# Kernel optimization log

Measured on AMD Instinct MI355X. Metric: run time of the kernel, lower is better.

## Reference

```python
import jax, jax.numpy as jnp
import numpy as np

MARGIN = 1.0


def setup_inputs() -> dict:
    key = jax.random.key(0)
    k1, k2, k3 = jax.random.split(key, 3)
    N, F = 4096, 512
    a = jax.random.normal(k1, (N, F), dtype=jnp.float32)
    b = jax.random.normal(k2, (N, F), dtype=jnp.float32)
    labels = jax.random.randint(k3, (N,), 0, 16, dtype=jnp.int32)
    return {"a": a, "b": b, "labels": labels}


def reference(a, b, labels):
    # D[i, j] = ||b_i - a_j||  (torch: Xa=a[None], Xb=b[:,None], sum over feat)
    # GEMM form of the pairwise sqdist; clamp tiny fp negatives before sqrt.
    Dsq = (jnp.sum(b * b, axis=1)[:, None]
           + jnp.sum(a * a, axis=1)[None, :]
           - 2.0 * (b @ a.T))
    D = jnp.sqrt(jnp.maximum(Dsq, 0.0))            # [N, N]
    Dexpm = jnp.exp(MARGIN - D)                    # [N, N]

    same = labels[:, None] == labels[None, :]      # [N, N]
    eye = jnp.eye(labels.shape[0], dtype=bool)
    pos_mask = same & ~eye                         # ordered positive pairs (i, j)
    neg_mask = ~same                               # negative pairs (labels differ)

    # neg_i sum for row i: sum_k Dexpm[i, k] over k with labels[k] != labels[i]
    row_negsum = jnp.sum(jnp.where(neg_mask, Dexpm, 0.0), axis=1)  # [N]

    # J_ij = log(neg_ik_sum + neg_jl_sum) + D[i, j]; hinged and squared
    J = jnp.log(row_negsum[:, None] + row_negsum[None, :]) + D
    hinge_sq = jnp.square(jnp.maximum(J, 0.0))

    num_pos = jnp.sum(pos_mask)
    return jnp.sum(jnp.where(pos_mask, hinge_sq, 0.0)) / (2.0 * num_pos)
```

## Files before the change

### kernel.cpp

```cpp
#include <hip/hip_runtime.h>
#include <math.h>

#define NROW 4096
#define FDIM 512
#define MARGIN 1.0f

typedef __attribute__((ext_vector_type(8))) short short8;
typedef __attribute__((ext_vector_type(4))) float floatx4;

__device__ inline unsigned short f2bf(float x) {
    unsigned u = __float_as_uint(x);
    return (unsigned short)((u + 0x7FFFu + ((u >> 16) & 1u)) >> 16);
}
__device__ inline float h2f(unsigned short u) {
    _Float16 h; __builtin_memcpy(&h, &u, 2); return (float)h;
}
__device__ inline unsigned short f2h(float f) {
    _Float16 h = (_Float16)f; unsigned short u; __builtin_memcpy(&u, &h, 2); return u;
}
__device__ inline void glds16(const unsigned short* g, unsigned short* l) {
    __builtin_amdgcn_global_load_lds(
        (const __attribute__((address_space(1))) unsigned int*)g,
        (__attribute__((address_space(3))) unsigned int*)l, 16, 0, 0);
}

__global__ __launch_bounds__(64) void prep_kernel(
    const float* __restrict__ a, const float* __restrict__ b,
    unsigned short* __restrict__ abf, unsigned short* __restrict__ bbf,
    float* __restrict__ na, float* __restrict__ nb,
    float* __restrict__ rns, float* __restrict__ loss) {
    int row  = blockIdx.x;
    int lane = threadIdx.x;
    const float4* a4 = (const float4*)(a + (size_t)row * FDIM);
    const float4* b4 = (const float4*)(b + (size_t)row * FDIM);
    ushort4* au = (ushort4*)(abf + (size_t)row * FDIM);
    ushort4* bu = (ushort4*)(bbf + (size_t)row * FDIM);
    float sa = 0.f, sb = 0.f;
    #pragma unroll
    for (int f = lane; f < FDIM / 4; f += 64) {
        float4 va = a4[f];
        float4 vb = b4[f];
        sa += va.x * va.x + va.y * va.y + va.z * va.z + va.w * va.w;
        sb += vb.x * vb.x + vb.y * vb.y + vb.z * vb.z + vb.w * vb.w;
        ushort4 ua = { f2bf(va.x), f2bf(va.y), f2bf(va.z), f2bf(va.w) };
        ushort4 ub = { f2bf(vb.x), f2bf(vb.y), f2bf(vb.z), f2bf(vb.w) };
        au[f] = ua;
        bu[f] = ub;
    }
    #pragma unroll
    for (int o = 32; o > 0; o >>= 1) {
        sa += __shfl_down(sa, o);
        sb += __shfl_down(sb, o);
    }
    if (lane == 0) {
        na[row] = sa;
        nb[row] = sb;
        rns[row] = 0.f;
        if (row == 0) loss[0] = 0.f;
    }
}

template <int MODE>
__global__ __launch_bounds__(256) void pass_mfma(
    const unsigned short* __restrict__ abf, const unsigned short* __restrict__ bbf,
    const int* __restrict__ labels,
    const float* __restrict__ na, const float* __restrict__ nb,
    float* __restrict__ rns, unsigned short* __restrict__ Dws,
    float* __restrict__ loss_sum)
{
    __shared__ __align__(16) unsigned short arena[16384];
    __shared__ int   li_s[128], lj_s[128];
    __shared__ float nb_s[128], na_s[128], rbi_s[128], rbj_s[128];

    const int t    = threadIdx.x;
    const int lane = t & 63;
    const int w    = t >> 6;
    const int wi   = w >> 1, wj = w & 1;
    const int bid  = blockIdx.x;
    const int sup  = bid >> 6, loc = bid & 63;
    const int by   = ((sup >> 2) << 3) | (loc >> 3);
    const int bx   = ((sup & 3) << 3) | (loc & 7);
    const int ti   = by * 128;
    const int tj   = bx * 128;
    const int lr   = lane & 15;
    const int lq   = lane >> 4;

    floatx4 acc[4][4];
    #pragma unroll
    for (int i = 0; i < 4; ++i)
        #pragma unroll
        for (int j = 0; j < 4; ++j)
            acc[i][j] = (floatx4){0.f, 0.f, 0.f, 0.f};

    if (t < 128) {
        li_s[t] = labels[ti + t];
        nb_s[t] = nb[ti + t];
        if (MODE == 2) rbi_s[t] = rns[ti + t];
    } else {
        int u = t - 128;
        lj_s[u] = labels[tj + u];
        na_s[u] = na[tj + u];
        if (MODE == 2) rbj_s[u] = rns[tj + u];
    }

    auto stage = [&](int kk, int buf) {
        unsigned short* As = arena + buf * 8192;
        unsigned short* Bs = arena + 4096 + buf * 8192;
        #pragma unroll
        for (int l = 0; l < 2; ++l) {
            int c   = t + l * 256;
            int row = c >> 2;
            int q   = c & 3;
            glds16(abf + (size_t)(tj + row) * FDIM + kk + q * 8, As + c * 8);
            glds16(bbf + (size_t)(ti + row) * FDIM + kk + q * 8, Bs + c * 8);
        }
    };

    stage(0, 0);
    __syncthreads();

    #pragma unroll
    for (int it = 0; it < FDIM / 32; ++it) {
        if (it < FDIM / 32 - 1) stage((it + 1) * 32, (it + 1) & 1);

        const unsigned short* As = arena + (it & 1) * 8192;
        const unsigned short* Bs = As + 4096;
        short8 af[4], bf[4];
        #pragma unroll
        for (int ri = 0; ri < 4; ++ri)
            af[ri] = *(const short8*)&Bs[(wi * 64 + ri * 16 + lr) * 32 + lq * 8];
        #pragma unroll
        for (int rj = 0; rj < 4; ++rj)
            bf[rj] = *(const short8*)&As[(wj * 64 + rj * 16 + lr) * 32 + lq * 8];
        #pragma unroll
        for (int ri = 0; ri < 4; ++ri)
            #pragma unroll
            for (int rj = 0; rj < 4; ++rj)
                acc[ri][rj] = __builtin_amdgcn_mfma_f32_16x16x32_bf16(
                    af[ri], bf[rj], acc[ri][rj], 0, 0, 0);
        __syncthreads();
    }

    if (MODE == 0 || MODE == 1) {
        unsigned short* dblk = Dws + (size_t)bid * 16384;
        #pragma unroll
        for (int ri = 0; ri < 4; ++ri) {
            float rs[4] = {0.f, 0.f, 0.f, 0.f};
            unsigned short dloc[16];
            #pragma unroll
            for (int rj = 0; rj < 4; ++rj) {
                int   jl  = wj * 64 + rj * 16 + lr;
                float naj = na_s[jl];
                int   ljv = lj_s[jl];
                #pragma unroll
                for (int r = 0; r < 4; ++r) {
                    int   il  = wi * 64 + ri * 16 + lq * 4 + r;
                    float dsq = nb_s[il] + naj - 2.f * acc[ri][rj][r];
                    float D   = sqrtf(fmaxf(dsq, 0.f));
                    if (li_s[il] != ljv) rs[r] += __expf(MARGIN - D);
                    if (MODE == 0) dloc[rj * 4 + r] = f2h(D);
                }
            }
            #pragma unroll
            for (int r = 0; r < 4; ++r) {
                #pragma unroll
                for (int o = 8; o > 0; o >>= 1) rs[r] += __shfl_down(rs[r], o, 16);
            }
            if (lr == 0) {
                #pragma unroll
                for (int r = 0; r < 4; ++r)
                    atomicAdd(&rns[ti + wi * 64 + ri * 16 + lq * 4 + r], rs[r]);
            }
            if (MODE == 0) {
                *(short8*)&dblk[(ri * 2 + 0) * 2048 + t * 8] = *(short8*)&dloc[0];
                *(short8*)&dblk[(ri * 2 + 1) * 2048 + t * 8] = *(short8*)&dloc[8];
            }
        }
    } else {
        float local = 0.f;
        #pragma unroll
        for (int ri = 0; ri < 4; ++ri)
            #pragma unroll
            for (int rj = 0; rj < 4; ++rj) {
                int jl  = wj * 64 + rj * 16 + lr;
                int ljv = lj_s[jl];
                float naj = na_s[jl], rbj = rbj_s[jl];
                #pragma unroll
                for (int r = 0; r < 4; ++r) {
                    int il = wi * 64 + ri * 16 + lq * 4 + r;
                    int i  = ti + il, j = tj + jl;
                    if (li_s[il] == ljv && i != j) {
                        float dsq = nb_s[il] + naj - 2.f * acc[ri][rj][r];
                        float D   = sqrtf(fmaxf(dsq, 0.f));
                        float J   = __logf(rbi_s[il] + rbj) + D;
                        float h   = fmaxf(J, 0.f);
                        local += h * h;
                    }
                }
            }
        #pragma unroll
        for (int o = 32; o > 0; o >>= 1) local += __shfl_down(local, o);
        __shared__ float part[4];
        if (lane == 0) part[w] = local;
        __syncthreads();
        if (t == 0) atomicAdd(loss_sum, part[0] + part[1] + part[2] + part[3]);
    }
}

__global__ __launch_bounds__(256) void pass2_sweep(
    const unsigned short* __restrict__ Dws, const int* __restrict__ labels,
    const float* __restrict__ rns, float* __restrict__ loss_sum)
{
    __shared__ int   lab_i[128], lab_j[128];
    __shared__ float rb_i[128], rb_j[128];

    const int t    = threadIdx.x;
    const int lane = t & 63;
    const int w    = t >> 6;
    const int wi   = w >> 1, wj = w & 1;
    const int bid  = blockIdx.x;
    const int sup  = bid >> 6, loc = bid & 63;
    const int by   = ((sup >> 2) << 3) | (loc >> 3);
    const int bx   = ((sup & 3) << 3) | (loc & 7);
    const int ti   = by * 128;
    const int tj   = bx * 128;
    const int lr   = lane & 15;
    const int lq   = lane >> 4;

    if (t < 128) {
        lab_i[t] = labels[ti + t];
        rb_i[t]  = rns[ti + t];
    } else {
        int u = t - 128;
        lab_j[u] = labels[tj + u];
        rb_j[u]  = rns[tj + u];
    }
    __syncthreads();

    const unsigned short* dblk = Dws + (size_t)bid * 16384;
    float local = 0.f;
    #pragma unroll
    for (int ri = 0; ri < 4; ++ri) {
        short8 d0 = *(const short8*)&dblk[(ri * 2 + 0) * 2048 + t * 8];
        short8 d1 = *(const short8*)&dblk[(ri * 2 + 1) * 2048 + t * 8];
        #pragma unroll
        for (int rj = 0; rj < 4; ++rj) {
            int jl  = wj * 64 + rj * 16 + lr;
            int ljv = lab_j[jl];
            #pragma unroll
            for (int r = 0; r < 4; ++r) {
                int il = wi * 64 + ri * 16 + lq * 4 + r;
                if (lab_i[il] == ljv && (ti + il) != (tj + jl)) {
                    unsigned short du = (rj < 2)
                        ? (unsigned short)d0[rj * 4 + r]
                        : (unsigned short)d1[(rj - 2) * 4 + r];
                    float J = __logf(rb_i[il] + rb_j[jl]) + h2f(du);
                    float h = fmaxf(J, 0.f);
                    local += h * h;
                }
            }
        }
    }
    #pragma unroll
    for (int o = 32; o > 0; o >>= 1) local += __shfl_down(local, o);
    __shared__ float part[4];
    if (lane == 0) part[w] = local;
    __syncthreads();
    if (t == 0) atomicAdd(loss_sum, part[0] + part[1] + part[2] + part[3]);
}

__global__ __launch_bounds__(256) void finalize_kernel(const int* __restrict__ labels,
                                                       const float* __restrict__ loss_sum,
                                                       float* __restrict__ out) {
    __shared__ int hist[16];
    int t = threadIdx.x;
    if (t < 16) hist[t] = 0;
    __syncthreads();
    for (int i = t; i < NROW; i += 256) atomicAdd(&hist[labels[i] & 15], 1);
    __syncthreads();
    if (t == 0) {
        long long np = 0;
        for (int c = 0; c < 16; ++c) np += (long long)hist[c] * (long long)(hist[c] - 1);
        out[0] = loss_sum[0] / (2.0f * (float)np);
    }
}

extern "C" void kernel_launch(void* const* d_in, const int* in_sizes, int n_in,
                              void* d_out, int out_size, void* d_ws, size_t ws_size,
                              hipStream_t stream) {
    const float* a      = (const float*)d_in[0];
    const float* b      = (const float*)d_in[1];
    const int*   labels = (const int*)d_in[2];
    float* out = (float*)d_out;

    unsigned short* abf = (unsigned short*)d_ws;
    unsigned short* bbf = abf + (size_t)NROW * FDIM;
    float* fws  = (float*)(bbf + (size_t)NROW * FDIM);
    float* na   = fws;
    float* nb   = fws + NROW;
    float* rns  = fws + 2 * NROW;
    float* loss = fws + 3 * NROW;
    unsigned short* Dws = (unsigned short*)(fws + 3 * NROW + 4);

    size_t need = ((char*)Dws - (char*)d_ws) + (size_t)NROW * NROW * 2;

    prep_kernel<<<NROW, 64, 0, stream>>>(a, b, abf, bbf, na, nb, rns, loss);

    dim3 grid((NROW / 128) * (NROW / 128));
    if (ws_size >= need) {
        pass_mfma<0><<<grid, 256, 0, stream>>>(abf, bbf, labels, na, nb, rns, Dws, loss);
        pass2_sweep<<<grid, 256, 0, stream>>>(Dws, labels, rns, loss);
    } else {
        pass_mfma<1><<<grid, 256, 0, stream>>>(abf, bbf, labels, na, nb, rns, Dws, loss);
        pass_mfma<2><<<grid, 256, 0, stream>>>(abf, bbf, labels, na, nb, rns, Dws, loss);
    }

    finalize_kernel<<<1, 256, 0, stream>>>(labels, loss, out);
}
```

Before: 135.1 us.

## Replace dense distance cache with label-grouped positive-pair GEMM pass

Stops writing the full fp16 distance matrix in the first pass and removes the dense second sweep. Rows are grouped by label (histogram plus permutation built in an extra prep block), and a work list of 64x64 same-label tiles is recomputed with a small MFMA GEMM over gathered rows. Only the roughly 1/16 of pairs that share a label are touched, and the last block folds in the finalize step. The cost is recomputing those dot products with a serial single-lane work-list build and gather-based loads.

```diff
diff --git a/kernel.cpp b/kernel.cpp
--- a/kernel.cpp
+++ b/kernel.cpp
@@ -4,6 +4,7 @@
 #define NROW 4096
 #define FDIM 512
 #define MARGIN 1.0f
+#define NLAB 16
 
 typedef __attribute__((ext_vector_type(8))) short short8;
 typedef __attribute__((ext_vector_type(4))) float floatx4;
@@ -11,12 +12,6 @@
 __device__ inline unsigned short f2bf(float x) {
     unsigned u = __float_as_uint(x);
     return (unsigned short)((u + 0x7FFFu + ((u >> 16) & 1u)) >> 16);
-}
-__device__ inline float h2f(unsigned short u) {
-    _Float16 h; __builtin_memcpy(&h, &u, 2); return (float)h;
-}
-__device__ inline unsigned short f2h(float f) {
-    _Float16 h = (_Float16)f; unsigned short u; __builtin_memcpy(&u, &h, 2); return u;
 }
 __device__ inline void glds16(const unsigned short* g, unsigned short* l) {
     __builtin_amdgcn_global_load_lds(
@@ -26,11 +21,50 @@
 
 __global__ __launch_bounds__(64) void prep_kernel(
     const float* __restrict__ a, const float* __restrict__ b,
+    const int* __restrict__ labels,
     unsigned short* __restrict__ abf, unsigned short* __restrict__ bbf,
     float* __restrict__ na, float* __restrict__ nb,
-    float* __restrict__ rns, float* __restrict__ loss) {
+    float* __restrict__ rns, float* __restrict__ loss,
+    int* __restrict__ perm, int* __restrict__ goff,
+    int* __restrict__ wl, int* __restrict__ wlmeta) {
     int row  = blockIdx.x;
     int lane = threadIdx.x;
+
+    if (row == NROW) {
+        __shared__ int hist[NLAB], off[NLAB], cur[NLAB];
+        if (lane < NLAB) hist[lane] = 0;
+        __syncthreads();
+        for (int i = lane; i < NROW; i += 64) atomicAdd(&hist[labels[i] & 15], 1);
+        __syncthreads();
+        if (lane == 0) {
+            int acc = 0;
+            for (int g = 0; g < NLAB; ++g) { off[g] = acc; acc += hist[g]; }
+            int n = 0;
+            int np = 0;
+            for (int g = 0; g < NLAB; ++g) {
+                goff[g] = off[g];
+                int c = hist[g];
+                np += c * (c - 1);
+                int nt = (c + 63) >> 6;
+                for (int ti = 0; ti < nt; ++ti)
+                    for (int tj = 0; tj < nt; ++tj)
+                        wl[n++] = (g << 12) | (ti << 6) | tj;
+            }
+            goff[NLAB] = NROW;
+            wlmeta[0] = n;
+            wlmeta[1] = np;
+            wlmeta[2] = 0;
+        }
+        __syncthreads();
+        if (lane < NLAB) cur[lane] = off[lane];
+        __syncthreads();
+        for (int i = lane; i < NROW; i += 64) {
+            int pos = atomicAdd(&cur[labels[i] & 15], 1);
+            perm[pos] = i;
+        }
+        return;
+    }
+
     const float4* a4 = (const float4*)(a + (size_t)row * FDIM);
     const float4* b4 = (const float4*)(b + (size_t)row * FDIM);
     ushort4* au = (ushort4*)(abf + (size_t)row * FDIM);
@@ -60,17 +94,15 @@
     }
 }
 
-template <int MODE>
-__global__ __launch_bounds__(256) void pass_mfma(
+__global__ __launch_bounds__(256) void pass_neg(
     const unsigned short* __restrict__ abf, const unsigned short* __restrict__ bbf,
     const int* __restrict__ labels,
     const float* __restrict__ na, const float* __restrict__ nb,
-    float* __restrict__ rns, unsigned short* __restrict__ Dws,
-    float* __restrict__ loss_sum)
+    float* __restrict__ rns)
 {
     __shared__ __align__(16) unsigned short arena[16384];
     __shared__ int   li_s[128], lj_s[128];
-    __shared__ float nb_s[128], na_s[128], rbi_s[128], rbj_s[128];
+    __shared__ float nb_s[128], na_s[128];
 
     const int t    = threadIdx.x;
     const int lane = t & 63;
@@ -95,12 +127,10 @@
     if (t < 128) {
         li_s[t] = labels[ti + t];
         nb_s[t] = nb[ti + t];
-        if (MODE == 2) rbi_s[t] = rns[ti + t];
     } else {
         int u = t - 128;
         lj_s[u] = labels[tj + u];
         na_s[u] = na[tj + u];
-        if (MODE == 2) rbj_s[u] = rns[tj + u];
     }
 
     auto stage = [&](int kk, int buf) {
@@ -141,56 +171,141 @@
         __syncthreads();
     }
 
-    if (MODE == 0 || MODE == 1) {
-        unsigned short* dblk = Dws + (size_t)bid * 16384;
-        #pragma unroll
-        for (int ri = 0; ri < 4; ++ri) {
-            float rs[4] = {0.f, 0.f, 0.f, 0.f};
-            unsigned short dloc[16];
-            #pragma unroll
-            for (int rj = 0; rj < 4; ++rj) {
-                int   jl  = wj * 64 + rj * 16 + lr;
-                float naj = na_s[jl];
-                int   ljv = lj_s[jl];
+    #pragma unroll
+    for (int ri = 0; ri < 4; ++ri) {
+        float rs[4] = {0.f, 0.f, 0.f, 0.f};
+        #pragma unroll
+        for (int rj = 0; rj < 4; ++rj) {
+            int   jl  = wj * 64 + rj * 16 + lr;
+            float naj = na_s[jl];
+            int   ljv = lj_s[jl];
+            #pragma unroll
+            for (int r = 0; r < 4; ++r) {
+                int il = wi * 64 + ri * 16 + lq * 4 + r;
+                if (li_s[il] != ljv) {
+                    float dsq = nb_s[il] + naj - 2.f * acc[ri][rj][r];
+                    float D   = sqrtf(fmaxf(dsq, 0.f));
+                    rs[r] += __expf(MARGIN - D);
+                }
+            }
+        }
+        #pragma unroll
+        for (int r = 0; r < 4; ++r) {
+            #pragma unroll
+            for (int o = 8; o > 0; o >>= 1) rs[r] += __shfl_down(rs[r], o, 16);
+        }
+        if (lr == 0) {
+            #pragma unroll
+            for (int r = 0; r < 4; ++r)
+                atomicAdd(&rns[ti + wi * 64 + ri * 16 + lq * 4 + r], rs[r]);
+        }
+    }
+}
+
+__global__ __launch_bounds__(256) void pass2_pos(
+    const unsigned short* __restrict__ abf, const unsigned short* __restrict__ bbf,
+    const float* __restrict__ na, const float* __restrict__ nb,
+    const float* __restrict__ rns,
+    const int* __restrict__ perm, const int* __restrict__ goff,
+    const int* __restrict__ wl, const int* __restrict__ wlmeta,
+    float* __restrict__ loss_sum, int* __restrict__ done,
+    float* __restrict__ out)
+{
+    __shared__ __align__(16) unsigned short arena[8192];
+    __shared__ int   rows_i[64], rows_j[64];
+    __shared__ float rbi_s[64], rbj_s[64], nbi_s[64], naj_s[64];
+    __shared__ float part[4];
+
+    const int t    = threadIdx.x;
+    const int lane = t & 63;
+    const int w    = t >> 6;
+    const int wi   = w >> 1, wj = w & 1;
+    const int lr   = lane & 15;
+    const int lq   = lane >> 4;
+    const int nwl  = wlmeta[0];
+
+    float local = 0.f;
+
+    for (int item = blockIdx.x; item < nwl; item += gridDim.x) {
+        __syncthreads();
+        int e  = wl[item];
+        int g  = e >> 12, ti = (e >> 6) & 63, tj = e & 63;
+        int gb = goff[g], ge = goff[g + 1];
+        int cnt = ge - gb;
+
+        if (t < 64) {
+            int idx = gb + ti * 64 + t;
+            int ig  = perm[idx < ge ? idx : gb];
+            rows_i[t] = ig;
+            rbi_s[t]  = rns[ig];
+            nbi_s[t]  = nb[ig];
+        } else if (t < 128) {
+            int u   = t - 64;
+            int idx = gb + tj * 64 + u;
+            int jg  = perm[idx < ge ? idx : gb];
+            rows_j[u] = jg;
+            rbj_s[u]  = rns[jg];
+            naj_s[u]  = na[jg];
+        }
+        __syncthreads();
+
+        int srow_a = rows_j[t >> 2];
+        int srow_b = rows_i[t >> 2];
+        int q      = t & 3;
+
+        floatx4 acc[2][2];
+        #pragma unroll
+        for (int i = 0; i < 2; ++i)
+            #pragma unroll
+            for (int j = 0; j < 2; ++j)
+                acc[i][j] = (floatx4){0.f, 0.f, 0.f, 0.f};
+
+        auto stage = [&](int kk, int buf) {
+            unsigned short* As = arena + buf * 4096;
+            unsigned short* Bs = As + 2048;
+            glds16(abf + (size_t)srow_a * FDIM + kk + q * 8, As + t * 8);
+            glds16(bbf + (size_t)srow_b * FDIM + kk + q * 8, Bs + t * 8);
+        };
+
+        stage(0, 0);
+        __syncthreads();
+
+        #pragma unroll
+        for (int itk = 0; itk < FDIM / 32; ++itk) {
+            if (itk < FDIM / 32 - 1) stage((itk + 1) * 32, (itk + 1) & 1);
+
+            const unsigned short* As = arena + (itk & 1) * 4096;
+            const unsigned short* Bs = As + 2048;
+            short8 af[2], bf[2];
+            #pragma unroll
+            for (int ri = 0; ri < 2; ++ri)
+                af[ri] = *(const short8*)&Bs[(wi * 32 + ri * 16 + lr) * 32 + lq * 8];
+            #pragma unroll
+            for (int rj = 0; rj < 2; ++rj)
+                bf[rj] = *(const short8*)&As[(wj * 32 + rj * 16 + lr) * 32 + lq * 8];
+            #pragma unroll
+            for (int ri = 0; ri < 2; ++ri)
+                #pragma unroll
+                for (int rj = 0; rj < 2; ++rj)
+                    acc[ri][rj] = __builtin_amdgcn_mfma_f32_16x16x32_bf16(
+                        af[ri], bf[rj], acc[ri][rj], 0, 0, 0);
+            __syncthreads();
+        }
+
+        #pragma unroll
+        for (int ri = 0; ri < 2; ++ri)
+            #pragma unroll
+            for (int rj = 0; rj < 2; ++rj) {
+                int  jl  = wj * 32 + rj * 16 + lr;
+                bool vj  = (tj * 64 + jl) < cnt;
+                int  jg  = rows_j[jl];
+                float nav = naj_s[jl], rbj = rbj_s[jl];
                 #pragma unroll
                 for (int r = 0; r < 4; ++r) {
-                    int   il  = wi * 64 + ri * 16 + lq * 4 + r;
-                    float dsq = nb_s[il] + naj - 2.f * acc[ri][rj][r];
-                    float D   = sqrtf(fmaxf(dsq, 0.f));
-                    if (li_s[il] != ljv) rs[r] += __expf(MARGIN - D);
-                    if (MODE == 0) dloc[rj * 4 + r] = f2h(D);
-                }
-            }
-            #pragma unroll
-            for (int r = 0; r < 4; ++r) {
-                #pragma unroll
-                for (int o = 8; o > 0; o >>= 1) rs[r] += __shfl_down(rs[r], o, 16);
-            }
-            if (lr == 0) {
-                #pragma unroll
-                for (int r = 0; r < 4; ++r)
-                    atomicAdd(&rns[ti + wi * 64 + ri * 16 + lq * 4 + r], rs[r]);
-            }
-            if (MODE == 0) {
-                *(short8*)&dblk[(ri * 2 + 0) * 2048 + t * 8] = *(short8*)&dloc[0];
-                *(short8*)&dblk[(ri * 2 + 1) * 2048 + t * 8] = *(short8*)&dloc[8];
-            }
-        }
-    } else {
-        float local = 0.f;
-        #pragma unroll
-        for (int ri = 0; ri < 4; ++ri)
-            #pragma unroll
-            for (int rj = 0; rj < 4; ++rj) {
-                int jl  = wj * 64 + rj * 16 + lr;
-                int ljv = lj_s[jl];
-                float naj = na_s[jl], rbj = rbj_s[jl];
-                #pragma unroll
-                for (int r = 0; r < 4; ++r) {
-                    int il = wi * 64 + ri * 16 + lq * 4 + r;
-                    int i  = ti + il, j = tj + jl;
-                    if (li_s[il] == ljv && i != j) {
-                        float dsq = nb_s[il] + naj - 2.f * acc[ri][rj][r];
+                    int  il = wi * 32 + ri * 16 + lq * 4 + r;
+                    bool vi = (ti * 64 + il) < cnt;
+                    if (vi && vj && rows_i[il] != jg) {
+                        float dsq = nbi_s[il] + nav - 2.f * acc[ri][rj][r];
                         float D   = sqrtf(fmaxf(dsq, 0.f));
                         float J   = __logf(rbi_s[il] + rbj) + D;
                         float h   = fmaxf(J, 0.f);
@@ -198,90 +313,21 @@
                     }
                 }
             }
-        #pragma unroll
-        for (int o = 32; o > 0; o >>= 1) local += __shfl_down(local, o);
-        __shared__ float part[4];
-        if (lane == 0) part[w] = local;
-        __syncthreads();
-        if (t == 0) atomicAdd(loss_sum, part[0] + part[1] + part[2] + part[3]);
-    }
-}
-
-__global__ __launch_bounds__(256) void pass2_sweep(
-    const unsigned short* __restrict__ Dws, const int* __restrict__ labels,
-    const float* __restrict__ rns, float* __restrict__ loss_sum)
-{
-    __shared__ int   lab_i[128], lab_j[128];
-    __shared__ float rb_i[128], rb_j[128];
-
-    const int t    = threadIdx.x;
-    const int lane = t & 63;
-    const int w    = t >> 6;
-    const int wi   = w >> 1, wj = w & 1;
-    const int bid  = blockIdx.x;
-    const int sup  = bid >> 6, loc = bid & 63;
-    const int by   = ((sup >> 2) << 3) | (loc >> 3);
-    const int bx   = ((sup & 3) << 3) | (loc & 7);
-    const int ti   = by * 128;
-    const int tj   = bx * 128;
-    const int lr   = lane & 15;
-    const int lq   = lane >> 4;
-
-    if (t < 128) {
-        lab_i[t] = labels[ti + t];
-        rb_i[t]  = rns[ti + t];
-    } else {
-        int u = t - 128;
-        lab_j[u] = labels[tj + u];
-        rb_j[u]  = rns[tj + u];
-    }
-    __syncthreads();
-
-    const unsigned short* dblk = Dws + (size_t)bid * 16384;
-    float local = 0.f;
-    #pragma unroll
-    for (int ri = 0; ri < 4; ++ri) {
-        short8 d0 = *(const short8*)&dblk[(ri * 2 + 0) * 2048 + t * 8];
-        short8 d1 = *(const short8*)&dblk[(ri * 2 + 1) * 2048 + t * 8];
-        #pragma unroll
-        for (int rj = 0; rj < 4; ++rj) {
-            int jl  = wj * 64 + rj * 16 + lr;
-            int ljv = lab_j[jl];
-            #pragma unroll
-            for (int r = 0; r < 4; ++r) {
-                int il = wi * 64 + ri * 16 + lq * 4 + r;
-                if (lab_i[il] == ljv && (ti + il) != (tj + jl)) {
-                    unsigned short du = (rj < 2)
-                        ? (unsigned short)d0[rj * 4 + r]
-                        : (unsigned short)d1[(rj - 2) * 4 + r];
-                    float J = __logf(rb_i[il] + rb_j[jl]) + h2f(du);
-                    float h = fmaxf(J, 0.f);
-                    local += h * h;
-                }
-            }
-        }
-    }
+    }
+
     #pragma unroll
     for (int o = 32; o > 0; o >>= 1) local += __shfl_down(local, o);
-    __shared__ float part[4];
     if (lane == 0) part[w] = local;
     __syncthreads();
-    if (t == 0) atomicAdd(loss_sum, part[0] + part[1] + part[2] + part[3]);
-}
-
-__global__ __launch_bounds__(256) void finalize_kernel(const int* __restrict__ labels,
-                                                       const float* __restrict__ loss_sum,
-                                                       float* __restrict__ out) {
-    __shared__ int hist[16];
-    int t = threadIdx.x;
-    if (t < 16) hist[t] = 0;
-    __syncthreads();
-    for (int i = t; i < NROW; i += 256) atomicAdd(&hist[labels[i] & 15], 1);
-    __syncthreads();
     if (t == 0) {
-        long long np = 0;
-        for (int c = 0; c < 16; ++c) np += (long long)hist[c] * (long long)(hist[c] - 1);
-        out[0] = loss_sum[0] / (2.0f * (float)np);
+        atomicAdd(loss_sum, part[0] + part[1] + part[2] + part[3]);
+        __threadfence();
+        int old = atomicAdd(done, 1);
+        if (old == (int)gridDim.x - 1) {
+            __threadfence();
+            float total = *(volatile float*)loss_sum;
+            out[0] = total / (2.0f * (float)wlmeta[1]);
+        }
     }
 }
 
@@ -300,20 +346,16 @@
     float* nb   = fws + NROW;
     float* rns  = fws + 2 * NROW;
     float* loss = fws + 3 * NROW;
-    unsigned short* Dws = (unsigned short*)(fws + 3 * NROW + 4);
-
-    size_t need = ((char*)Dws - (char*)d_ws) + (size_t)NROW * NROW * 2;
-
-    prep_kernel<<<NROW, 64, 0, stream>>>(a, b, abf, bbf, na, nb, rns, loss);
-
-    dim3 grid((NROW / 128) * (NROW / 128));
-    if (ws_size >= need) {
-        pass_mfma<0><<<grid, 256, 0, stream>>>(abf, bbf, labels, na, nb, rns, Dws, loss);
-        pass2_sweep<<<grid, 256, 0, stream>>>(Dws, labels, rns, loss);
-    } else {
-        pass_mfma<1><<<grid, 256, 0, stream>>>(abf, bbf, labels, na, nb, rns, Dws, loss);
-        pass_mfma<2><<<grid, 256, 0, stream>>>(abf, bbf, labels, na, nb, rns, Dws, loss);
-    }
-
-    finalize_kernel<<<1, 256, 0, stream>>>(labels, loss, out);
-}
+    int* iws    = (int*)(fws + 3 * NROW + 4);
+    int* perm   = iws;
+    int* goff   = iws + NROW;
+    int* wlmeta = iws + NROW + 20;
+    int* wl     = iws + NROW + 24;
+
+    prep_kernel<<<NROW + 1, 64, 0, stream>>>(a, b, labels, abf, bbf, na, nb,
+                                             rns, loss, perm, goff, wl, wlmeta);
+    pass_neg<<<(NROW / 128) * (NROW / 128), 256, 0, stream>>>(abf, bbf, labels,
+                                                              na, nb, rns);
+    pass2_pos<<<256, 256, 0, stream>>>(abf, bbf, na, nb, rns, perm, goff, wl,
+                                       wlmeta, loss, &wlmeta[2], out);
+}
```

Result: slower. 169.4 us (+25.4%).
